# Kernel optimization log

Hardware: AMD Instinct MI355X
Metric: run time of the kernel (lower is better)

Reference implementation:

```python
import jax, jax.numpy as jnp
import numpy as np

N_NODES = 50000
N_EDGES = 800000
D = 64


def setup_inputs() -> dict:
    key = jax.random.key(0)
    k = jax.random.split(key, 8)
    h = jax.random.normal(k[0], (N_NODES, D), dtype=jnp.float32)
    edge_src = jax.random.randint(k[1], (N_EDGES,), 0, N_NODES, dtype=jnp.int32)
    edge_dst = jax.random.randint(k[2], (N_EDGES,), 0, N_NODES, dtype=jnp.int32)
    # normalized adjacency weights (e.g. 1/deg style values in (0,1))
    edge_w = jax.random.uniform(k[3], (N_EDGES,), dtype=jnp.float32)
    W_self = jax.random.normal(k[4], (D, D), dtype=jnp.float32) / np.sqrt(D)
    b_self = jnp.zeros((D,), dtype=jnp.float32)
    W_neigh = jax.random.normal(k[5], (D, D), dtype=jnp.float32) / np.sqrt(D)
    b_neigh = jnp.zeros((D,), dtype=jnp.float32)
    return {
        "h": h,
        "edge_src": edge_src,
        "edge_dst": edge_dst,
        "edge_w": edge_w,
        "W_self": W_self,
        "b_self": b_self,
        "W_neigh": W_neigh,
        "b_neigh": b_neigh,
    }


def reference(h, edge_src, edge_dst, edge_w, W_self, b_self, W_neigh, b_neigh):
    # neigh = A_norm @ h : sparse COO matmul as weighted gather + segment-sum
    # messages: [E, D]
    msgs = edge_w[:, None] * h[edge_src]
    neigh = jax.ops.segment_sum(msgs, edge_dst, num_segments=N_NODES)  # [N, D]
    # out = lin_self(h) + lin_neigh(neigh), relu; dropout is a no-op in eval mode
    out = (h @ W_self.T + b_self) + (neigh @ W_neigh.T + b_neigh)
    return jax.nn.relu(out)
```

## Files before the change

### kernel.cpp

```cpp
#include <hip/hip_runtime.h>

#define N_NODES 50000
#define N_EDGES 800000
#define D 64

#define NPB 200
#define NB  250
#define CAP 4096
#define BT  512
#define EPT 4
#define CHUNK_E (BT * EPT)
#define NCHUNKS ((N_EDGES + CHUNK_E - 1) / CHUNK_E)
#define CT  1024
#define GBLK 16

typedef unsigned short ushort_t;
typedef unsigned int   uint_t;
typedef __attribute__((ext_vector_type(8))) short   short8;
typedef __attribute__((ext_vector_type(4))) float   float4v;

__device__ __forceinline__ ushort_t f2b(float f) {
    uint_t u = __float_as_uint(f);
    return (ushort_t)((u + 0x7FFFu + ((u >> 16) & 1u)) >> 16);
}
__device__ __forceinline__ float b2f(ushort_t b) {
    return __uint_as_float((uint_t)b << 16);
}
__device__ __forceinline__ float lane_bcast(float v, int l) {
    return __int_as_float(__builtin_amdgcn_readlane(__float_as_int(v), l));
}


__global__ __launch_bounds__(BT) void bin_h2b_kernel(
    const int* __restrict__ src, const int* __restrict__ dst,
    const float* __restrict__ w, int* __restrict__ cursor,
    int2* __restrict__ bedges,
    const float* __restrict__ h, ushort_t* __restrict__ hb)
{
    if (blockIdx.x >= NCHUNKS) {
        const int nb = gridDim.x - NCHUNKS;
        for (int i = (blockIdx.x - NCHUNKS) * BT + threadIdx.x;
             i < N_NODES * D / 4; i += nb * BT) {
            const float4 v = ((const float4*)h)[i];
            ushort4 o;
            o.x = f2b(v.x); o.y = f2b(v.y); o.z = f2b(v.z); o.w = f2b(v.w);
            ((ushort4*)hb)[i] = o;
        }
        return;
    }

    __shared__ int lh[NB];
    __shared__ int loff[NB];
    __shared__ int lcur[NB];
    __shared__ int gpos[NB];
    __shared__ int part[256];
    __shared__ int2 stage[CHUNK_E];
    __shared__ unsigned char sbk[CHUNK_E];

    const int t = threadIdx.x;
    for (int i = t; i < NB; i += BT) lh[i] = 0;
    __syncthreads();

    const int base = blockIdx.x * CHUNK_E;
    int   my_b[EPT];
    int   my_p[EPT];
    float my_w[EPT];
#pragma unroll
    for (int k = 0; k < EPT; ++k) {
        const int e = base + k * BT + t;
        if (e < N_EDGES) {
            const int d = dst[e];
            const int b = (unsigned)d / NPB;
            my_b[k] = b;
            my_p[k] = (src[e] << 8) | (d - b * NPB);
            my_w[k] = w[e];
            atomicAdd(&lh[b], 1);
        } else {
            my_b[k] = -1;
        }
    }
    __syncthreads();

    const int v = (t < NB) ? lh[t] : 0;
    if (t < 256) part[t] = v;
    __syncthreads();
    for (int off = 1; off < 256; off <<= 1) {
        int p = 0;
        if (t < 256 && t >= off) p = part[t - off];
        __syncthreads();
        if (t < 256) part[t] += p;
        __syncthreads();
    }
    if (t < NB) { loff[t] = part[t] - v; lcur[t] = part[t] - v; }
    __syncthreads();

#pragma unroll
    for (int k = 0; k < EPT; ++k) {
        if (my_b[k] >= 0) {
            const int p = atomicAdd(&lcur[my_b[k]], 1);
            stage[p] = make_int2(my_p[k], __float_as_int(my_w[k]));
            sbk[p] = (unsigned char)my_b[k];
        }
    }
    __syncthreads();

    if (t < NB && lh[t] > 0)
        gpos[t] = t * CAP + atomicAdd(&cursor[t], lh[t]);
    __syncthreads();

    const int tot = min(N_EDGES - base, CHUNK_E);
    for (int s = t; s < tot; s += BT) {
        const int b = sbk[s];
        bedges[gpos[b] + (s - loff[b])] = stage[s];
    }
}

__global__ __launch_bounds__(CT) void bucket_csr_kernel(
    const int* __restrict__ cursor, int2* __restrict__ edges,
    int2* __restrict__ offs2)
{
    __shared__ int  lcur[NPB];
    __shared__ int  part[256];
    __shared__ int2 stage[CAP];

    const int b   = blockIdx.x;
    const int t   = threadIdx.x;
    const int gb  = b * CAP;
    const int cnt = min(cursor[b], CAP);

    if (t < NPB) lcur[t] = 0;
    __syncthreads();
    for (int e = t; e < cnt; e += CT)
        atomicAdd(&lcur[edges[gb + e].x & 255], 1);
    __syncthreads();

    const int v = (t < NPB) ? lcur[t] : 0;
    if (t < 256) part[t] = v;
    __syncthreads();
    for (int off = 1; off < 256; off <<= 1) {
        int p = 0;
        if (t < 256 && t >= off) p = part[t - off];
        __syncthreads();
        if (t < 256) part[t] += p;
        __syncthreads();
    }
    if (t < NPB) {
        const int ex = part[t] - v;
        lcur[t] = ex;
        offs2[b * NPB + t] = make_int2(gb + ex, gb + ex + v);
    }
    __syncthreads();

    for (int e = t; e < cnt; e += CT) {
        const int2 r = edges[gb + e];
        const int p = atomicAdd(&lcur[r.x & 255], 1);
        stage[p] = make_int2(r.x >> 8, r.y);
    }
    __syncthreads();
    for (int s = t; s < cnt; s += CT)
        edges[gb + s] = stage[s];
}

__global__ __launch_bounds__(512) void gather_linear_kernel(
    const ushort_t* __restrict__ hb, const int2* __restrict__ edges,
    const int2* __restrict__ offs2,
    const float* __restrict__ Ws, const float* __restrict__ bs,
    const float* __restrict__ Wn, const float* __restrict__ bn,
    float* __restrict__ out)
{
    __shared__ ushort_t nstage[GBLK * D];

    const int wave  = threadIdx.x >> 6;
    const int lane  = threadIdx.x & 63;
    const int node0 = blockIdx.x * GBLK;

#pragma unroll
    for (int jj = 0; jj < 2; ++jj) {
        const int j = wave * 2 + jj;
        const int node = node0 + j;
        if (node < N_NODES) {
            const int2 be = offs2[node];
            const int beg = be.x, end = be.y;
            float acc = 0.f;
            int e = beg;
            for (; e + 8 <= end; e += 8) {
                int2  r[8];
                float vv[8];
#pragma unroll
                for (int k = 0; k < 8; ++k) r[k] = edges[e + k];
#pragma unroll
                for (int k = 0; k < 8; ++k) vv[k] = b2f(hb[(size_t)r[k].x * D + lane]);
#pragma unroll
                for (int k = 0; k < 8; ++k) acc = fmaf(__int_as_float(r[k].y), vv[k], acc);
            }
            for (; e + 4 <= end; e += 4) {
                const int2 e0 = edges[e], e1 = edges[e + 1], e2 = edges[e + 2], e3 = edges[e + 3];
                const float v0 = b2f(hb[(size_t)e0.x * D + lane]);
                const float v1 = b2f(hb[(size_t)e1.x * D + lane]);
                const float v2 = b2f(hb[(size_t)e2.x * D + lane]);
                const float v3 = b2f(hb[(size_t)e3.x * D + lane]);
                acc = fmaf(__int_as_float(e0.y), v0, acc);
                acc = fmaf(__int_as_float(e1.y), v1, acc);
                acc = fmaf(__int_as_float(e2.y), v2, acc);
                acc = fmaf(__int_as_float(e3.y), v3, acc);
            }
            for (; e < end; ++e) {
                const int2 r = edges[e];
                acc = fmaf(__int_as_float(r.y), b2f(hb[(size_t)r.x * D + lane]), acc);
            }
            nstage[j * D + lane] = f2b(acc);
        }
    }
    __syncthreads();

    const int nt = wave;
    if (nt >= 4 || node0 >= N_NODES) return;
    const int row16 = lane & 15;
    const int quad  = lane >> 4;

    const size_t abase = (size_t)(node0 + row16) * D + quad * 8;
    const short8 ah0 = *(const short8*)(hb + abase);
    const short8 ah1 = *(const short8*)(hb + abase + 32);
    const ushort_t* sp = nstage + row16 * D + quad * 8;
    const short8 an0 = *(const short8*)sp;
    const short8 an1 = *(const short8*)(sp + 32);

    const int col = nt * 16 + row16;
    const float* wsr = Ws + (size_t)col * D + quad * 8;
    const float* wnr = Wn + (size_t)col * D + quad * 8;
    short8 bw[4];
#pragma unroll
    for (int f = 0; f < 4; ++f) {
        const float* p = (f < 2 ? wsr : wnr) + (f & 1) * 32;
        const float4 w0 = *(const float4*)p;
        const float4 w1 = *(const float4*)(p + 4);
        short8 bwv;
        bwv[0] = (short)f2b(w0.x); bwv[1] = (short)f2b(w0.y);
        bwv[2] = (short)f2b(w0.z); bwv[3] = (short)f2b(w0.w);
        bwv[4] = (short)f2b(w1.x); bwv[5] = (short)f2b(w1.y);
        bwv[6] = (short)f2b(w1.z); bwv[7] = (short)f2b(w1.w);
        bw[f] = bwv;
    }
    float4v acc = {0.f, 0.f, 0.f, 0.f};
    acc = __builtin_amdgcn_mfma_f32_16x16x32_bf16(ah0, bw[0], acc, 0, 0, 0);
    acc = __builtin_amdgcn_mfma_f32_16x16x32_bf16(ah1, bw[1], acc, 0, 0, 0);
    acc = __builtin_amdgcn_mfma_f32_16x16x32_bf16(an0, bw[2], acc, 0, 0, 0);
    acc = __builtin_amdgcn_mfma_f32_16x16x32_bf16(an1, bw[3], acc, 0, 0, 0);

    const float bias = bs[col] + bn[col];
#pragma unroll
    for (int r = 0; r < 4; ++r) {
        const int m = quad * 4 + r;
        out[(size_t)(node0 + m) * D + col] = fmaxf(acc[r] + bias, 0.f);
    }
}

__global__ __launch_bounds__(256) void sage_scatter(
    const float* __restrict__ h,
    const int* __restrict__ edge_src,
    const int* __restrict__ edge_dst,
    const float* __restrict__ edge_w,
    float* __restrict__ neigh)
{
    const long long tid = (long long)blockIdx.x * blockDim.x + threadIdx.x;
    const int e = (int)(tid >> 6);
    const int d = (int)(tid & 63);
    if (e >= N_EDGES) return;
    atomicAdd(&neigh[(long long)edge_dst[e] * D + d],
              edge_w[e] * h[(long long)edge_src[e] * D + d]);
}

__global__ __launch_bounds__(256, 2) void linear_f32_kernel(
    const float* __restrict__ h, const float* __restrict__ neigh,
    const float* __restrict__ Ws, const float* __restrict__ bs,
    const float* __restrict__ Wn, const float* __restrict__ bn,
    float* __restrict__ out)
{
    const int lane   = threadIdx.x & 63;
    const int gwave  = (blockIdx.x * blockDim.x + threadIdx.x) >> 6;
    const int nwaves = (gridDim.x * blockDim.x) >> 6;

    float Wsr[D], Wnr[D];
#pragma unroll
    for (int k = 0; k < D; k += 4) {
        const float4 a = *(const float4*)&Ws[(size_t)lane * D + k];
        const float4 b = *(const float4*)&Wn[(size_t)lane * D + k];
        Wsr[k] = a.x; Wsr[k+1] = a.y; Wsr[k+2] = a.z; Wsr[k+3] = a.w;
        Wnr[k] = b.x; Wnr[k+1] = b.y; Wnr[k+2] = b.z; Wnr[k+3] = b.w;
    }
    const float bias = bs[lane] + bn[lane];

    for (int n = gwave; n < N_NODES; n += nwaves) {
        const float hv = h[(size_t)n * D + lane];
        const float nv = neigh[(size_t)n * D + lane];
        float o = bias;
#pragma unroll
        for (int k = 0; k < D; ++k) {
            o = fmaf(lane_bcast(hv, k), Wsr[k], o);
            o = fmaf(lane_bcast(nv, k), Wnr[k], o);
        }
        out[(size_t)n * D + lane] = fmaxf(o, 0.f);
    }
}

extern "C" void kernel_launch(void* const* d_in, const int* in_sizes, int n_in,
                              void* d_out, int out_size, void* d_ws, size_t ws_size,
                              hipStream_t stream)
{
    const float* h        = (const float*)d_in[0];
    const int*   edge_src = (const int*)d_in[1];
    const int*   edge_dst = (const int*)d_in[2];
    const float* edge_w   = (const float*)d_in[3];
    const float* W_self   = (const float*)d_in[4];
    const float* b_self   = (const float*)d_in[5];
    const float* W_neigh  = (const float*)d_in[6];
    const float* b_neigh  = (const float*)d_in[7];
    float*       out      = (float*)d_out;

    int2*     edges  = (int2*)d_ws;
    int2*     offs2  = edges + (size_t)NB * CAP;
    ushort_t* hb     = (ushort_t*)(offs2 + N_NODES);
    int*      cursor = (int*)(hb + (size_t)N_NODES * D);
    const size_t needed = (size_t)NB * CAP * 8 + (size_t)N_NODES * 8
                        + (size_t)N_NODES * D * 2 + NB * 4;

    if (ws_size >= needed) {
        hipMemsetAsync(cursor, 0, NB * sizeof(int), stream);
        bin_h2b_kernel<<<NCHUNKS * 2, BT, 0, stream>>>(
            edge_src, edge_dst, edge_w, cursor, edges, h, hb);
        bucket_csr_kernel<<<NB, CT, 0, stream>>>(cursor, edges, offs2);
        gather_linear_kernel<<<(N_NODES + GBLK - 1) / GBLK, 512, 0, stream>>>(
            hb, edges, offs2, W_self, b_self, W_neigh, b_neigh, out);
    } else {
        float* neigh_fb = (float*)d_ws;
        hipMemsetAsync(neigh_fb, 0, (size_t)N_NODES * D * sizeof(float), stream);
        const long long total = (long long)N_EDGES * 64;
        sage_scatter<<<(int)((total + 255) / 256), 256, 0, stream>>>(
            h, edge_src, edge_dst, edge_w, neigh_fb);
        linear_f32_kernel<<<1024, 256, 0, stream>>>(h, neigh_fb, W_self, b_self,
                                                    W_neigh, b_neigh, out);
    }
}
```

Baseline: 147.3 us.

## Pack CSR edges into 32-bit src index plus bf16 weight, unroll gather 16

The bucket CSR kernel now writes each edge as one 32-bit word: a 16-bit source index in the low half and a round-to-nearest bf16 weight in the high half. It writes into a separate output buffer rather than rewriting the binned buffer in place. The gather kernel reads these packed words, which halves the edge-stream bytes, and its main loop is unrolled from 8 to 16 edges to keep more loads in flight. The cost is extra workspace, bf16 rounding of the edge weights, and a hard limit that node ids must fit in 16 bits.

```diff
diff --git a/kernel.cpp b/kernel.cpp
--- a/kernel.cpp
+++ b/kernel.cpp
@@ -25,6 +25,9 @@
 }
 __device__ __forceinline__ float b2f(ushort_t b) {
     return __uint_as_float((uint_t)b << 16);
+}
+__device__ __forceinline__ uint_t rne_hi16(uint_t u) {
+    return (u + 0x7FFFu + ((u >> 16) & 1u)) & 0xFFFF0000u;
 }
 __device__ __forceinline__ float lane_bcast(float v, int l) {
     return __int_as_float(__builtin_amdgcn_readlane(__float_as_int(v), l));
@@ -116,12 +119,12 @@
 }
 
 __global__ __launch_bounds__(CT) void bucket_csr_kernel(
-    const int* __restrict__ cursor, int2* __restrict__ edges,
-    int2* __restrict__ offs2)
-{
-    __shared__ int  lcur[NPB];
-    __shared__ int  part[256];
-    __shared__ int2 stage[CAP];
+    const int* __restrict__ cursor, const int2* __restrict__ bedges,
+    uint_t* __restrict__ pedges, int2* __restrict__ offs2)
+{
+    __shared__ int    lcur[NPB];
+    __shared__ int    part[256];
+    __shared__ uint_t stage[CAP];
 
     const int b   = blockIdx.x;
     const int t   = threadIdx.x;
@@ -131,7 +134,7 @@
     if (t < NPB) lcur[t] = 0;
     __syncthreads();
     for (int e = t; e < cnt; e += CT)
-        atomicAdd(&lcur[edges[gb + e].x & 255], 1);
+        atomicAdd(&lcur[bedges[gb + e].x & 255], 1);
     __syncthreads();
 
     const int v = (t < NPB) ? lcur[t] : 0;
@@ -152,17 +155,17 @@
     __syncthreads();
 
     for (int e = t; e < cnt; e += CT) {
-        const int2 r = edges[gb + e];
+        const int2 r = bedges[gb + e];
         const int p = atomicAdd(&lcur[r.x & 255], 1);
-        stage[p] = make_int2(r.x >> 8, r.y);
+        stage[p] = (uint_t)(r.x >> 8) | rne_hi16((uint_t)r.y);
     }
     __syncthreads();
     for (int s = t; s < cnt; s += CT)
-        edges[gb + s] = stage[s];
+        pedges[gb + s] = stage[s];
 }
 
 __global__ __launch_bounds__(512) void gather_linear_kernel(
-    const ushort_t* __restrict__ hb, const int2* __restrict__ edges,
+    const ushort_t* __restrict__ hb, const uint_t* __restrict__ pedges,
     const int2* __restrict__ offs2,
     const float* __restrict__ Ws, const float* __restrict__ bs,
     const float* __restrict__ Wn, const float* __restrict__ bn,
@@ -183,30 +186,34 @@
             const int beg = be.x, end = be.y;
             float acc = 0.f;
             int e = beg;
-            for (; e + 8 <= end; e += 8) {
-                int2  r[8];
-                float vv[8];
-#pragma unroll
-                for (int k = 0; k < 8; ++k) r[k] = edges[e + k];
-#pragma unroll
-                for (int k = 0; k < 8; ++k) vv[k] = b2f(hb[(size_t)r[k].x * D + lane]);
-#pragma unroll
-                for (int k = 0; k < 8; ++k) acc = fmaf(__int_as_float(r[k].y), vv[k], acc);
+            for (; e + 16 <= end; e += 16) {
+                uint_t r[16];
+                float  vv[16];
+#pragma unroll
+                for (int k = 0; k < 16; ++k) r[k] = pedges[e + k];
+#pragma unroll
+                for (int k = 0; k < 16; ++k)
+                    vv[k] = b2f(hb[(size_t)(r[k] & 0xFFFFu) * D + lane]);
+#pragma unroll
+                for (int k = 0; k < 16; ++k)
+                    acc = fmaf(__uint_as_float(r[k] & 0xFFFF0000u), vv[k], acc);
             }
             for (; e + 4 <= end; e += 4) {
-                const int2 e0 = edges[e], e1 = edges[e + 1], e2 = edges[e + 2], e3 = edges[e + 3];
-                const float v0 = b2f(hb[(size_t)e0.x * D + lane]);
-                const float v1 = b2f(hb[(size_t)e1.x * D + lane]);
-                const float v2 = b2f(hb[(size_t)e2.x * D + lane]);
-                const float v3 = b2f(hb[(size_t)e3.x * D + lane]);
-                acc = fmaf(__int_as_float(e0.y), v0, acc);
-                acc = fmaf(__int_as_float(e1.y), v1, acc);
-                acc = fmaf(__int_as_float(e2.y), v2, acc);
-                acc = fmaf(__int_as_float(e3.y), v3, acc);
+                uint_t r[4];
+                float  vv[4];
+#pragma unroll
+                for (int k = 0; k < 4; ++k) r[k] = pedges[e + k];
+#pragma unroll
+                for (int k = 0; k < 4; ++k)
+                    vv[k] = b2f(hb[(size_t)(r[k] & 0xFFFFu) * D + lane]);
+#pragma unroll
+                for (int k = 0; k < 4; ++k)
+                    acc = fmaf(__uint_as_float(r[k] & 0xFFFF0000u), vv[k], acc);
             }
             for (; e < end; ++e) {
-                const int2 r = edges[e];
-                acc = fmaf(__int_as_float(r.y), b2f(hb[(size_t)r.x * D + lane]), acc);
+                const uint_t r = pedges[e];
+                acc = fmaf(__uint_as_float(r & 0xFFFF0000u),
+                           b2f(hb[(size_t)(r & 0xFFFFu) * D + lane]), acc);
             }
             nstage[j * D + lane] = f2b(acc);
         }
@@ -317,20 +324,21 @@
     const float* b_neigh  = (const float*)d_in[7];
     float*       out      = (float*)d_out;
 
-    int2*     edges  = (int2*)d_ws;
-    int2*     offs2  = edges + (size_t)NB * CAP;
+    int2*     bedges = (int2*)d_ws;
+    uint_t*   pedges = (uint_t*)(bedges + (size_t)NB * CAP);
+    int2*     offs2  = (int2*)(pedges + (size_t)NB * CAP);
     ushort_t* hb     = (ushort_t*)(offs2 + N_NODES);
     int*      cursor = (int*)(hb + (size_t)N_NODES * D);
-    const size_t needed = (size_t)NB * CAP * 8 + (size_t)N_NODES * 8
-                        + (size_t)N_NODES * D * 2 + NB * 4;
+    const size_t needed = (size_t)NB * CAP * 8 + (size_t)NB * CAP * 4
+                        + (size_t)N_NODES * 8 + (size_t)N_NODES * D * 2 + NB * 4;
 
     if (ws_size >= needed) {
         hipMemsetAsync(cursor, 0, NB * sizeof(int), stream);
         bin_h2b_kernel<<<NCHUNKS * 2, BT, 0, stream>>>(
-            edge_src, edge_dst, edge_w, cursor, edges, h, hb);
-        bucket_csr_kernel<<<NB, CT, 0, stream>>>(cursor, edges, offs2);
+            edge_src, edge_dst, edge_w, cursor, bedges, h, hb);
+        bucket_csr_kernel<<<NB, CT, 0, stream>>>(cursor, bedges, pedges, offs2);
         gather_linear_kernel<<<(N_NODES + GBLK - 1) / GBLK, 512, 0, stream>>>(
-            hb, edges, offs2, W_self, b_self, W_neigh, b_neigh, out);
+            hb, pedges, offs2, W_self, b_self, W_neigh, b_neigh, out);
     } else {
         float* neigh_fb = (float*)d_ws;
         hipMemsetAsync(neigh_fb, 0, (size_t)N_NODES * D * sizeof(float), stream);
```

Measured after the change: 145.1 us (median of 2 runs). No clear change (-1.5%).

## Drop per-bucket CSR sort; accumulate bucket neighbors in LDS with atomics

Applied to the files above, without the earlier changes.

The second pass that sorted each bucket's edges by destination is removed. Edges are still binned into smaller buckets, and the gather kernel now runs one block per bucket. That block accumulates weighted messages into a shared-memory fp32 tile using LDS atomics, then applies the two linear layers with MFMA directly from that tile. This saves a kernel launch plus a global read/write pass over all edges. In exchange it adds LDS atomic contention and gives only 511 blocks of 1024 threads. It also depends on 16-bit packing of the source index and on bucket capacity limits.

```diff
diff --git a/kernel.cpp b/kernel.cpp
--- a/kernel.cpp
+++ b/kernel.cpp
@@ -4,15 +4,15 @@
 #define N_EDGES 800000
 #define D 64
 
-#define NPB 200
-#define NB  250
-#define CAP 4096
+#define NPB 98
+#define NB  511
+#define CAP 1920
+#define ACC_ROWS 112
 #define BT  512
 #define EPT 4
 #define CHUNK_E (BT * EPT)
 #define NCHUNKS ((N_EDGES + CHUNK_E - 1) / CHUNK_E)
-#define CT  1024
-#define GBLK 16
+#define GT  1024
 
 typedef unsigned short ushort_t;
 typedef unsigned int   uint_t;
@@ -53,9 +53,9 @@
     __shared__ int loff[NB];
     __shared__ int lcur[NB];
     __shared__ int gpos[NB];
-    __shared__ int part[256];
+    __shared__ int part[BT];
     __shared__ int2 stage[CHUNK_E];
-    __shared__ unsigned char sbk[CHUNK_E];
+    __shared__ ushort_t sbk[CHUNK_E];
 
     const int t = threadIdx.x;
     for (int i = t; i < NB; i += BT) lh[i] = 0;
@@ -72,7 +72,7 @@
             const int d = dst[e];
             const int b = (unsigned)d / NPB;
             my_b[k] = b;
-            my_p[k] = (src[e] << 8) | (d - b * NPB);
+            my_p[k] = ((d - b * NPB) << 16) | src[e];
             my_w[k] = w[e];
             atomicAdd(&lh[b], 1);
         } else {
@@ -82,13 +82,12 @@
     __syncthreads();
 
     const int v = (t < NB) ? lh[t] : 0;
-    if (t < 256) part[t] = v;
-    __syncthreads();
-    for (int off = 1; off < 256; off <<= 1) {
-        int p = 0;
-        if (t < 256 && t >= off) p = part[t - off];
+    part[t] = v;
+    __syncthreads();
+    for (int off = 1; off < BT; off <<= 1) {
+        int p = (t >= off) ? part[t - off] : 0;
         __syncthreads();
-        if (t < 256) part[t] += p;
+        part[t] += p;
         __syncthreads();
     }
     if (t < NB) { loff[t] = part[t] - v; lcur[t] = part[t] - v; }
@@ -99,7 +98,7 @@
         if (my_b[k] >= 0) {
             const int p = atomicAdd(&lcur[my_b[k]], 1);
             stage[p] = make_int2(my_p[k], __float_as_int(my_w[k]));
-            sbk[p] = (unsigned char)my_b[k];
+            sbk[p] = (ushort_t)my_b[k];
         }
     }
     __syncthreads();
@@ -115,143 +114,103 @@
     }
 }
 
-__global__ __launch_bounds__(CT) void bucket_csr_kernel(
-    const int* __restrict__ cursor, int2* __restrict__ edges,
-    int2* __restrict__ offs2)
-{
-    __shared__ int  lcur[NPB];
-    __shared__ int  part[256];
-    __shared__ int2 stage[CAP];
-
-    const int b   = blockIdx.x;
-    const int t   = threadIdx.x;
-    const int gb  = b * CAP;
-    const int cnt = min(cursor[b], CAP);
-
-    if (t < NPB) lcur[t] = 0;
-    __syncthreads();
-    for (int e = t; e < cnt; e += CT)
-        atomicAdd(&lcur[edges[gb + e].x & 255], 1);
-    __syncthreads();
-
-    const int v = (t < NPB) ? lcur[t] : 0;
-    if (t < 256) part[t] = v;
-    __syncthreads();
-    for (int off = 1; off < 256; off <<= 1) {
-        int p = 0;
-        if (t < 256 && t >= off) p = part[t - off];
-        __syncthreads();
-        if (t < 256) part[t] += p;
-        __syncthreads();
-    }
-    if (t < NPB) {
-        const int ex = part[t] - v;
-        lcur[t] = ex;
-        offs2[b * NPB + t] = make_int2(gb + ex, gb + ex + v);
-    }
-    __syncthreads();
-
-    for (int e = t; e < cnt; e += CT) {
-        const int2 r = edges[gb + e];
-        const int p = atomicAdd(&lcur[r.x & 255], 1);
-        stage[p] = make_int2(r.x >> 8, r.y);
-    }
-    __syncthreads();
-    for (int s = t; s < cnt; s += CT)
-        edges[gb + s] = stage[s];
-}
-
-__global__ __launch_bounds__(512) void gather_linear_kernel(
-    const ushort_t* __restrict__ hb, const int2* __restrict__ edges,
-    const int2* __restrict__ offs2,
+__global__ __launch_bounds__(GT) void gather_linear_kernel(
+    const ushort_t* __restrict__ hb, const int2* __restrict__ bedges,
+    const int* __restrict__ cursor,
     const float* __restrict__ Ws, const float* __restrict__ bs,
     const float* __restrict__ Wn, const float* __restrict__ bn,
     float* __restrict__ out)
 {
-    __shared__ ushort_t nstage[GBLK * D];
-
-    const int wave  = threadIdx.x >> 6;
-    const int lane  = threadIdx.x & 63;
-    const int node0 = blockIdx.x * GBLK;
-
-#pragma unroll
-    for (int jj = 0; jj < 2; ++jj) {
-        const int j = wave * 2 + jj;
-        const int node = node0 + j;
-        if (node < N_NODES) {
-            const int2 be = offs2[node];
-            const int beg = be.x, end = be.y;
-            float acc = 0.f;
-            int e = beg;
-            for (; e + 8 <= end; e += 8) {
-                int2  r[8];
-                float vv[8];
-#pragma unroll
-                for (int k = 0; k < 8; ++k) r[k] = edges[e + k];
-#pragma unroll
-                for (int k = 0; k < 8; ++k) vv[k] = b2f(hb[(size_t)r[k].x * D + lane]);
-#pragma unroll
-                for (int k = 0; k < 8; ++k) acc = fmaf(__int_as_float(r[k].y), vv[k], acc);
-            }
-            for (; e + 4 <= end; e += 4) {
-                const int2 e0 = edges[e], e1 = edges[e + 1], e2 = edges[e + 2], e3 = edges[e + 3];
-                const float v0 = b2f(hb[(size_t)e0.x * D + lane]);
-                const float v1 = b2f(hb[(size_t)e1.x * D + lane]);
-                const float v2 = b2f(hb[(size_t)e2.x * D + lane]);
-                const float v3 = b2f(hb[(size_t)e3.x * D + lane]);
-                acc = fmaf(__int_as_float(e0.y), v0, acc);
-                acc = fmaf(__int_as_float(e1.y), v1, acc);
-                acc = fmaf(__int_as_float(e2.y), v2, acc);
-                acc = fmaf(__int_as_float(e3.y), v3, acc);
-            }
-            for (; e < end; ++e) {
-                const int2 r = edges[e];
-                acc = fmaf(__int_as_float(r.y), b2f(hb[(size_t)r.x * D + lane]), acc);
-            }
-            nstage[j * D + lane] = f2b(acc);
-        }
-    }
-    __syncthreads();
-
-    const int nt = wave;
-    if (nt >= 4 || node0 >= N_NODES) return;
-    const int row16 = lane & 15;
-    const int quad  = lane >> 4;
-
-    const size_t abase = (size_t)(node0 + row16) * D + quad * 8;
-    const short8 ah0 = *(const short8*)(hb + abase);
-    const short8 ah1 = *(const short8*)(hb + abase + 32);
-    const ushort_t* sp = nstage + row16 * D + quad * 8;
-    const short8 an0 = *(const short8*)sp;
-    const short8 an1 = *(const short8*)(sp + 32);
-
-    const int col = nt * 16 + row16;
-    const float* wsr = Ws + (size_t)col * D + quad * 8;
-    const float* wnr = Wn + (size_t)col * D + quad * 8;
-    short8 bw[4];
-#pragma unroll
-    for (int f = 0; f < 4; ++f) {
-        const float* p = (f < 2 ? wsr : wnr) + (f & 1) * 32;
-        const float4 w0 = *(const float4*)p;
-        const float4 w1 = *(const float4*)(p + 4);
-        short8 bwv;
-        bwv[0] = (short)f2b(w0.x); bwv[1] = (short)f2b(w0.y);
-        bwv[2] = (short)f2b(w0.z); bwv[3] = (short)f2b(w0.w);
-        bwv[4] = (short)f2b(w1.x); bwv[5] = (short)f2b(w1.y);
-        bwv[6] = (short)f2b(w1.z); bwv[7] = (short)f2b(w1.w);
-        bw[f] = bwv;
-    }
-    float4v acc = {0.f, 0.f, 0.f, 0.f};
-    acc = __builtin_amdgcn_mfma_f32_16x16x32_bf16(ah0, bw[0], acc, 0, 0, 0);
-    acc = __builtin_amdgcn_mfma_f32_16x16x32_bf16(ah1, bw[1], acc, 0, 0, 0);
-    acc = __builtin_amdgcn_mfma_f32_16x16x32_bf16(an0, bw[2], acc, 0, 0, 0);
-    acc = __builtin_amdgcn_mfma_f32_16x16x32_bf16(an1, bw[3], acc, 0, 0, 0);
-
-    const float bias = bs[col] + bn[col];
-#pragma unroll
-    for (int r = 0; r < 4; ++r) {
-        const int m = quad * 4 + r;
-        out[(size_t)(node0 + m) * D + col] = fmaxf(acc[r] + bias, 0.f);
+    __shared__ float acc[ACC_ROWS * D];
+
+    const int b    = blockIdx.x;
+    const int t    = threadIdx.x;
+    const int wave = t >> 6;
+    const int lane = t & 63;
+
+    for (int i = t; i < ACC_ROWS * D; i += GT) acc[i] = 0.f;
+    __syncthreads();
+
+    const int cnt = min(cursor[b], CAP);
+    const int gb  = b * CAP;
+    const int per = (cnt + (GT / 64) - 1) / (GT / 64);
+    const int e0  = wave * per;
+    const int e1  = min(e0 + per, cnt);
+
+    int e = e0;
+    for (; e + 8 <= e1; e += 8) {
+        int2  r[8];
+        float v[8];
+#pragma unroll
+        for (int k = 0; k < 8; ++k) r[k] = bedges[gb + e + k];
+#pragma unroll
+        for (int k = 0; k < 8; ++k)
+            v[k] = b2f(hb[(size_t)(r[k].x & 0xFFFF) * D + lane]);
+#pragma unroll
+        for (int k = 0; k < 8; ++k)
+            atomicAdd(&acc[(r[k].x >> 16) * D + lane],
+                      __int_as_float(r[k].y) * v[k]);
+    }
+    for (; e < e1; ++e) {
+        const int2 r = bedges[gb + e];
+        atomicAdd(&acc[(r.x >> 16) * D + lane],
+                  __int_as_float(r.y) * b2f(hb[(size_t)(r.x & 0xFFFF) * D + lane]));
+    }
+    __syncthreads();
+
+    const int bstart   = b * NPB;
+    const int nloc_end = min(NPB, N_NODES - bstart);
+    const int ngroups  = (nloc_end + 15) >> 4;
+    const int row16    = lane & 15;
+    const int quad     = lane >> 4;
+
+    for (int job = wave; job < ngroups * 4; job += GT / 64) {
+        const int ng = job >> 2;
+        const int ct = job & 3;
+        const int n0 = bstart + ng * 16;
+
+        const int arow = min(n0 + row16, N_NODES - 1);
+        const size_t abase = (size_t)arow * D + quad * 8;
+        const short8 ah0 = *(const short8*)(hb + abase);
+        const short8 ah1 = *(const short8*)(hb + abase + 32);
+        const int nl = ng * 16 + row16;
+        short8 an0, an1;
+#pragma unroll
+        for (int k = 0; k < 8; ++k)
+            an0[k] = (short)f2b(acc[nl * D + quad * 8 + k]);
+#pragma unroll
+        for (int k = 0; k < 8; ++k)
+            an1[k] = (short)f2b(acc[nl * D + 32 + quad * 8 + k]);
+
+        const int col = ct * 16 + row16;
+        const float* wsr = Ws + (size_t)col * D + quad * 8;
+        const float* wnr = Wn + (size_t)col * D + quad * 8;
+        short8 bw[4];
+#pragma unroll
+        for (int f = 0; f < 4; ++f) {
+            const float* p = (f < 2 ? wsr : wnr) + (f & 1) * 32;
+            const float4 w0 = *(const float4*)p;
+            const float4 w1 = *(const float4*)(p + 4);
+            short8 bwv;
+            bwv[0] = (short)f2b(w0.x); bwv[1] = (short)f2b(w0.y);
+            bwv[2] = (short)f2b(w0.z); bwv[3] = (short)f2b(w0.w);
+            bwv[4] = (short)f2b(w1.x); bwv[5] = (short)f2b(w1.y);
+            bwv[6] = (short)f2b(w1.z); bwv[7] = (short)f2b(w1.w);
+            bw[f] = bwv;
+        }
+        float4v c = {0.f, 0.f, 0.f, 0.f};
+        c = __builtin_amdgcn_mfma_f32_16x16x32_bf16(ah0, bw[0], c, 0, 0, 0);
+        c = __builtin_amdgcn_mfma_f32_16x16x32_bf16(ah1, bw[1], c, 0, 0, 0);
+        c = __builtin_amdgcn_mfma_f32_16x16x32_bf16(an0, bw[2], c, 0, 0, 0);
+        c = __builtin_amdgcn_mfma_f32_16x16x32_bf16(an1, bw[3], c, 0, 0, 0);
+
+        const float bias = bs[col] + bn[col];
+#pragma unroll
+        for (int r = 0; r < 4; ++r) {
+            const int nli = ng * 16 + quad * 4 + r;
+            if (nli < nloc_end)
+                out[(size_t)(bstart + nli) * D + col] = fmaxf(c[r] + bias, 0.f);
+        }
     }
 }
 
@@ -317,20 +276,17 @@
     const float* b_neigh  = (const float*)d_in[7];
     float*       out      = (float*)d_out;
 
-    int2*     edges  = (int2*)d_ws;
-    int2*     offs2  = edges + (size_t)NB * CAP;
-    ushort_t* hb     = (ushort_t*)(offs2 + N_NODES);
+    int2*     bedges = (int2*)d_ws;
+    ushort_t* hb     = (ushort_t*)(bedges + (size_t)NB * CAP);
     int*      cursor = (int*)(hb + (size_t)N_NODES * D);
-    const size_t needed = (size_t)NB * CAP * 8 + (size_t)N_NODES * 8
-                        + (size_t)N_NODES * D * 2 + NB * 4;
+    const size_t needed = (size_t)NB * CAP * 8 + (size_t)N_NODES * D * 2 + NB * 4;
 
     if (ws_size >= needed) {
         hipMemsetAsync(cursor, 0, NB * sizeof(int), stream);
         bin_h2b_kernel<<<NCHUNKS * 2, BT, 0, stream>>>(
-            edge_src, edge_dst, edge_w, cursor, edges, h, hb);
-        bucket_csr_kernel<<<NB, CT, 0, stream>>>(cursor, edges, offs2);
-        gather_linear_kernel<<<(N_NODES + GBLK - 1) / GBLK, 512, 0, stream>>>(
-            hb, edges, offs2, W_self, b_self, W_neigh, b_neigh, out);
+            edge_src, edge_dst, edge_w, cursor, bedges, h, hb);
+        gather_linear_kernel<<<NB, GT, 0, stream>>>(
+            hb, bedges, cursor, W_self, b_self, W_neigh, b_neigh, out);
     } else {
         float* neigh_fb = (float*)d_ws;
         hipMemsetAsync(neigh_fb, 0, (size_t)N_NODES * D * sizeof(float), stream);
```

Result: slower. 375.7 us (+155.0%).
